# Optimization experiments

Hardware: AMD Instinct MI355X
Metric: run time of the kernel (lower is better)

## Reference

```python
import jax, jax.numpy as jnp
import numpy as np

N, H, W, C = 8, 64, 64, 256
GC = 8            # channels per group (gc)
G = C // GC       # groups = 32
K = 3             # deformable kernel size
KK = K * K
DK = 3            # depthwise kernel size for offset/mask branch


def setup_inputs() -> dict:
    key = jax.random.key(0)
    ks = jax.random.split(key, 6)
    s = 0.02
    return {
        "x": jax.random.normal(ks[0], (N, H, W, C), jnp.float32),
        "dw_w": jax.random.normal(ks[1], (DK, DK, 1, C), jnp.float32) * s,
        "dw_b": jnp.zeros((C,), jnp.float32),
        "om_w": jax.random.normal(ks[2], (C, G * KK * 3), jnp.float32) * s,
        "om_b": jnp.zeros((G * KK * 3,), jnp.float32),
        "vp_w": jax.random.normal(ks[3], (C, C), jnp.float32) * s,
        "vp_b": jnp.zeros((C,), jnp.float32),
        "op_w": jax.random.normal(ks[4], (C, C), jnp.float32) * s,  # output_bias=False
    }


def _dcnv4(x, dw_w, dw_b, om_w, om_b, vp_w, vp_b, op_w):
    n, h, w, c = x.shape
    # --- offset/mask branch: depthwise conv then pointwise linear ---
    xdw = jax.lax.conv_general_dilated(
        x, dw_w, window_strides=(1, 1), padding="SAME",
        dimension_numbers=("NHWC", "HWIO", "NHWC"), feature_group_count=c) + dw_b
    om = (xdw @ om_w + om_b).reshape(n, h, w, G, KK * 3)
    offset = om[..., : 2 * KK].reshape(n, h, w, G, KK, 2)  # (dx, dy) per point
    mask = om[..., 2 * KK :]                                # [n,h,w,G,KK], raw (no softmax in v4)

    # --- value projection ---
    value = (x @ vp_w + vp_b).reshape(n, h, w, G, GC)

    # --- sampling locations: pixel + kernel-grid point + learned offset ---
    kg = (jnp.arange(K) - (K - 1) // 2).astype(jnp.float32)
    ky = jnp.repeat(kg, K)   # [KK]
    kx = jnp.tile(kg, K)     # [KK]
    base_y = jnp.arange(h, dtype=jnp.float32).reshape(1, h, 1, 1, 1)
    base_x = jnp.arange(w, dtype=jnp.float32).reshape(1, 1, w, 1, 1)
    py = base_y + ky + offset[..., 1]  # [n,h,w,G,KK]
    px = base_x + kx + offset[..., 0]

    y0 = jnp.floor(py)
    x0 = jnp.floor(px)
    ty = py - y0
    tx = px - x0

    n_idx = jnp.arange(n).reshape(n, 1, 1, 1, 1)
    g_idx = jnp.arange(G).reshape(1, 1, 1, G, 1)

    def gather(yi, xi):
        valid = (yi >= 0) & (yi <= h - 1) & (xi >= 0) & (xi <= w - 1)
        yc = jnp.clip(yi, 0, h - 1).astype(jnp.int32)
        xc = jnp.clip(xi, 0, w - 1).astype(jnp.int32)
        v = value[n_idx, yc, xc, g_idx]          # [n,h,w,G,KK,GC]
        return v * valid[..., None].astype(value.dtype)

    v00 = gather(y0, x0)
    v01 = gather(y0, x0 + 1)
    v10 = gather(y0 + 1, x0)
    v11 = gather(y0 + 1, x0 + 1)

    sampled = ((1 - ty) * (1 - tx))[..., None] * v00 \
            + ((1 - ty) * tx)[..., None] * v01 \
            + (ty * (1 - tx))[..., None] * v10 \
            + (ty * tx)[..., None] * v11        # [n,h,w,G,KK,GC]

    out = jnp.einsum("nhwgkc,nhwgk->nhwgc", sampled, mask).reshape(n, h, w, c)
    return out @ op_w                            # output proj, no bias


def reference(x, dw_w, dw_b, om_w, om_b, vp_w, vp_b, op_w):
    return _dcnv4(x, dw_w, dw_b, om_w, om_b, vp_w, vp_b, op_w)
```

## Files before the change

kernel.cpp:

```cpp
#include <hip/hip_runtime.h>


typedef __bf16 bf16_t;
typedef bf16_t bf16x8 __attribute__((ext_vector_type(8)));
typedef bf16_t bf16x4 __attribute__((ext_vector_type(4)));
typedef float f32x4 __attribute__((ext_vector_type(4)));

namespace {
constexpr int NN = 8, HH = 64, WW = 64, CC = 256;
constexpr int G = 32, GC = 8;
constexpr int NPIX = NN * HH * WW;
}

__device__ __forceinline__ size_t fragIdx(int row, int c) {
  return ((size_t)(row >> 4) * 4096) + ((c >> 5) * 512) + (((c >> 3) & 3) * 128) +
         ((row & 15) * 8) + (c & 7);
}

__global__ __launch_bounds__(256) void convert_weights_kernel(
    const float* __restrict__ om_w, const float* __restrict__ vp_w,
    const float* __restrict__ op_w, bf16_t* __restrict__ om_wG,
    bf16_t* __restrict__ vp_wF, bf16_t* __restrict__ op_wF) {
  __shared__ float s_t[64][65];
  __shared__ float s_w[256][27];
  const int b = blockIdx.x, t = threadIdx.x;
  if (b < 32) {
    const float* src;
    bf16_t* dst;
    int kt, nt;
    if (b < 16) { src = vp_w; dst = vp_wF; kt = b >> 2; nt = b & 3; }
    else        { src = op_w; dst = op_wF; kt = (b - 16) >> 2; nt = (b - 16) & 3; }
    const int nl = t & 63, kh = t >> 6;
    const int n = nt * 64 + nl;
#pragma unroll
    for (int i = 0; i < 16; ++i) {
      const int kl = kh * 16 + i;
      s_t[kl][nl] = src[(size_t)(kt * 64 + kl) * CC + n];
    }
    __syncthreads();
    const int lane = t & 63, kq = lane >> 4, n15 = lane & 15, n16 = t >> 6;
#pragma unroll
    for (int it = 0; it < 2; ++it) {
      bf16x8 v;
#pragma unroll
      for (int j = 0; j < 8; ++j)
        v[j] = (bf16_t)s_t[it * 32 + kq * 8 + j][n16 * 16 + n15];
      const size_t off = (size_t)(nt * 4 + n16) * 4096 + (size_t)(kt * 2 + it) * 512 +
                         kq * 128 + n15 * 8;
      *(bf16x8*)(dst + off) = v;
    }
  } else {
    const int g = b - 32;
#pragma unroll
    for (int j = 0; j < 27; ++j) s_w[t][j] = om_w[(size_t)t * 864 + g * 27 + j];
    __syncthreads();
#pragma unroll
    for (int i = 0; i < 4; ++i) {
      const int chunk = i * 256 + t;
      const int tile = chunk >> 9, ks = (chunk >> 6) & 7, kq = (chunk >> 4) & 3,
                n15 = chunk & 15;
      const int j = tile * 16 + n15;
      bf16x8 v;
#pragma unroll
      for (int cl = 0; cl < 8; ++cl) {
        const int c = ks * 32 + kq * 8 + cl;
        v[cl] = (j < 27) ? (bf16_t)s_w[c][j] : (bf16_t)0.0f;
      }
      *(bf16x8*)(om_wG + ((size_t)g << 13) + (size_t)chunk * 8) = v;
    }
  }
}

__global__ __launch_bounds__(512, 4) void dwconv_value_kernel(
    const float* __restrict__ x, const float* __restrict__ dw_w,
    const float* __restrict__ dw_b, const bf16_t* __restrict__ vp_wF,
    const float* __restrict__ vp_b, bf16_t* __restrict__ xdwF,
    bf16_t* __restrict__ value_g) {
  __shared__ bf16_t s_xf[64 * 256];

  const int t = threadIdx.x;
  const int row = blockIdx.x;
  const int y = row & 63;
  const int img = row >> 6;

  {
    const int cq = (t & 63) * 4;
    const int seg = t >> 6;
    const bool up = (y > 0), dn = (y < HH - 1);
    const float* xrow = x + (size_t)row * WW * CC + cq;

    const float4 bias = *(const float4*)&dw_b[cq];
    float4 dw[9];
#pragma unroll
    for (int i = 0; i < 9; ++i) dw[i] = *(const float4*)&dw_w[(size_t)i * CC + cq];

    const float4 zero = make_float4(0.f, 0.f, 0.f, 0.f);
    auto loadcol = [&](int xx, float4 c[3]) {
      if (xx < 0 || xx >= WW) { c[0] = c[1] = c[2] = zero; return; }
      c[0] = up ? *(const float4*)(xrow + ((size_t)xx - WW) * CC) : zero;
      c[1] = *(const float4*)(xrow + (size_t)xx * CC);
      c[2] = dn ? *(const float4*)(xrow + ((size_t)xx + WW) * CC) : zero;
    };

    const int x0 = seg * 8;
    float4 cm[3], cc[3], cp[3];
    loadcol(x0 - 1, cm);
    loadcol(x0, cc);

    for (int xx = x0; xx < x0 + 8; ++xx) {
      loadcol(xx + 1, cp);
      float4 a = bias;
#pragma unroll
      for (int r = 0; r < 3; ++r) {
        const float4 w0 = dw[r * 3 + 0], w1 = dw[r * 3 + 1], w2 = dw[r * 3 + 2];
        a.x = fmaf(cm[r].x, w0.x, fmaf(cc[r].x, w1.x, fmaf(cp[r].x, w2.x, a.x)));
        a.y = fmaf(cm[r].y, w0.y, fmaf(cc[r].y, w1.y, fmaf(cp[r].y, w2.y, a.y)));
        a.z = fmaf(cm[r].z, w0.z, fmaf(cc[r].z, w1.z, fmaf(cp[r].z, w2.z, a.z)));
        a.w = fmaf(cm[r].w, w0.w, fmaf(cc[r].w, w1.w, fmaf(cp[r].w, w2.w, a.w)));
      }
      const int pix = row * WW + xx;
      bf16x4 av, cv;
      av[0] = (bf16_t)a.x; av[1] = (bf16_t)a.y; av[2] = (bf16_t)a.z; av[3] = (bf16_t)a.w;
      cv[0] = (bf16_t)cc[1].x; cv[1] = (bf16_t)cc[1].y;
      cv[2] = (bf16_t)cc[1].z; cv[3] = (bf16_t)cc[1].w;
      *(bf16x4*)&xdwF[fragIdx(pix, cq)] = av;
      const int lf = (xx >> 4) * 4096 + ((cq >> 5) * 512) + (((cq >> 3) & 3) * 128) +
                     ((xx & 15) * 8) + (cq & 7);
      *(bf16x4*)&s_xf[lf] = cv;
#pragma unroll
      for (int r = 0; r < 3; ++r) { cm[r] = cc[r]; cc[r] = cp[r]; }
    }
  }
  __syncthreads();

  {
    const int lane = t & 63;
    const int wave = t >> 6;
    const int mq = wave >> 1;
    const int nh = wave & 1;
    const int m = lane & 15;
    const int kq = lane >> 4;

    const bf16_t* Ap = s_xf + mq * 4096 + lane * 8;
    const bf16_t* Bp = vp_wF + (size_t)(nh * 8) * 4096 + lane * 8;

    f32x4 acc[8] = {};
#pragma unroll
    for (int ks = 0; ks < 8; ++ks) {
      const bf16x8 a = *(const bf16x8*)(Ap + ks * 512);
#pragma unroll
      for (int i = 0; i < 8; ++i) {
        const bf16x8 b = *(const bf16x8*)(Bp + (size_t)i * 4096 + ks * 512);
        acc[i] = __builtin_amdgcn_mfma_f32_16x16x32_bf16(a, b, acc[i], 0, 0, 0);
      }
    }

#pragma unroll
    for (int i = 0; i < 8; ++i) {
      const int n = (nh * 8 + i) * 16 + m;
      const float bs = vp_b[n];
      const int g = n >> 3, c = n & 7;
      bf16_t* plane = value_g + ((size_t)(img * G + g) << 15) + c;
#pragma unroll
      for (int r = 0; r < 4; ++r) {
        const int pl = mq * 16 + kq * 4 + r;
        const int pin = y * 64 + pl;
        plane[(size_t)pin * GC] = (bf16_t)(acc[i][r] + bs);
      }
    }
  }
}

__global__ __launch_bounds__(512, 2) void oms_kernel(
    const bf16_t* __restrict__ xdwF, const bf16_t* __restrict__ om_wG,
    const float* __restrict__ om_b, const bf16_t* __restrict__ value_g,
    bf16_t* __restrict__ sampledF) {
  __shared__ bf16x8 s_v[66 * 66];
  __shared__ bf16_t s_om[8][4][128][8];

  const int t = threadIdx.x;
  const int lane = t & 63, wave = t >> 6;
  const int b = blockIdx.x;
  const int img = b & 7, g = (b >> 3) & 31, quarter = b >> 8;
  const int c15 = lane & 15, kq = lane >> 4;
  const int tile0 = img * 256 + quarter * 64;

  bf16x8 wf[2][8];
  {
    const bf16_t* base = om_wG + ((size_t)g << 13) + (size_t)lane * 8;
#pragma unroll
    for (int n2 = 0; n2 < 2; ++n2)
#pragma unroll
      for (int ks = 0; ks < 8; ++ks)
        wf[n2][ks] = *(const bf16x8*)(base + n2 * 4096 + ks * 512);
  }
  float bias[2][4];
#pragma unroll
  for (int n2 = 0; n2 < 2; ++n2)
#pragma unroll
    for (int r = 0; r < 4; ++r) {
      const int j = n2 * 16 + kq * 4 + r;
      bias[n2][r] = (j < 27) ? om_b[g * 27 + j] : 0.0f;
    }

  {
    const bf16x8 zv = {};
    for (int i = t; i < 260; i += 512) {
      int Y, X;
      if (i < 66)       { Y = 0;           X = i; }
      else if (i < 132) { Y = 65;          X = i - 66; }
      else if (i < 196) { Y = i - 132 + 1; X = 0; }
      else              { Y = i - 196 + 1; X = 65; }
      s_v[Y * 66 + X] = zv;
    }
    const bf16x8* plane = (const bf16x8*)(value_g + ((size_t)(img * G + g) << 15));
#pragma unroll
    for (int i = 0; i < 8; ++i) {
      const int c = i * 512 + t;
      s_v[((c >> 6) + 1) * 66 + (c & 63) + 1] = plane[c];
    }
  }

  {
    const int tb = tile0 + wave * 8;
#pragma unroll
    for (int q = 0; q < 8; ++q) {
      const bf16_t* Ap = xdwF + ((size_t)(tb + q)) * 4096 + (size_t)lane * 8;
      f32x4 a0 = {}, a1 = {};
#pragma unroll
      for (int ks = 0; ks < 8; ++ks) {
        const bf16x8 xf = *(const bf16x8*)(Ap + ks * 512);
        a0 = __builtin_amdgcn_mfma_f32_16x16x32_bf16(wf[0][ks], xf, a0, 0, 0, 0);
        a1 = __builtin_amdgcn_mfma_f32_16x16x32_bf16(wf[1][ks], xf, a1, 0, 0, 0);
      }
      const int p = q * 16 + c15;
      bf16x4 b0, b1;
#pragma unroll
      for (int r = 0; r < 4; ++r) {
        b0[r] = (bf16_t)(a0[r] + bias[0][r]);
        b1[r] = (bf16_t)(a1[r] + bias[1][r]);
      }
      *(bf16x4*)&s_om[wave][kq >> 1][p][(kq & 1) * 4] = b0;
      *(bf16x4*)&s_om[wave][2 + (kq >> 1)][p][(kq & 1) * 4] = b1;
    }
  }
  __syncthreads();

  {
    const int pinA = quarter * 1024 + wave * 128 + lane;
    const int pinB = pinA + 64;
    float arrA[27], arrB[27];
#pragma unroll
    for (int c = 0; c < 4; ++c) {
      const bf16x8 oA = *(const bf16x8*)&s_om[wave][c][lane][0];
      const bf16x8 oB = *(const bf16x8*)&s_om[wave][c][64 + lane][0];
#pragma unroll
      for (int j = 0; j < 8; ++j) {
        const int idx = c * 8 + j;
        if (idx < 27) { arrA[idx] = (float)oA[j]; arrB[idx] = (float)oB[j]; }
      }
    }
    const int xw = lane;
    const int yA = (pinA >> 6) & 63;
    const int yB = yA + 1;

    float accA[GC], accB[GC];
#pragma unroll
    for (int c = 0; c < GC; ++c) { accA[c] = 0.0f; accB[c] = 0.0f; }

    auto tap = [&](const float* arr, const int y, float* acc, const int k) {
      const float pxf = (float)(xw + (k % 3) - 1) + arr[2 * k];
      const float pyf = (float)(y + (k / 3) - 1) + arr[2 * k + 1];
      const float mk = arr[18 + k];
      const float x0f = floorf(pxf), y0f = floorf(pyf);
      const float tx = pxf - x0f, ty = pyf - y0f;
      const int ix = (int)x0f, iy = (int)y0f;

      const int iX0 = min(max(ix, -1), 64) + 1;
      const int iX1 = min(max(ix + 1, -1), 64) + 1;
      const int iY0 = min(max(iy, -1), 64) + 1;
      const int iY1 = min(max(iy + 1, -1), 64) + 1;

      const bf16x8 v00 = s_v[iY0 * 66 + iX0];
      const bf16x8 v01 = s_v[iY0 * 66 + iX1];
      const bf16x8 v10 = s_v[iY1 * 66 + iX0];
      const bf16x8 v11 = s_v[iY1 * 66 + iX1];

      const float w00 = mk * (1.0f - ty) * (1.0f - tx);
      const float w01 = mk * (1.0f - ty) * tx;
      const float w10 = mk * ty * (1.0f - tx);
      const float w11 = mk * ty * tx;

#pragma unroll
      for (int c = 0; c < GC; ++c) {
        float s = acc[c];
        s = fmaf(w00, (float)v00[c], s);
        s = fmaf(w01, (float)v01[c], s);
        s = fmaf(w10, (float)v10[c], s);
        s = fmaf(w11, (float)v11[c], s);
        acc[c] = s;
      }
    };

#pragma unroll
    for (int k = 0; k < 9; ++k) {
      tap(arrA, yA, accA, k);
      tap(arrB, yB, accB, k);
    }

    bf16x8 svA, svB;
#pragma unroll
    for (int c = 0; c < GC; ++c) {
      svA[c] = (bf16_t)accA[c];
      svB[c] = (bf16_t)accB[c];
    }
    *(bf16x8*)(sampledF + fragIdx(img * 4096 + pinA, g * 8)) = svA;
    *(bf16x8*)(sampledF + fragIdx(img * 4096 + pinB, g * 8)) = svB;
  }
}

__global__ __launch_bounds__(1024, 1) void out_gemm_kernel(
    const bf16_t* __restrict__ AF, const bf16_t* __restrict__ BF,
    float* __restrict__ out) {
  __shared__ bf16_t s_b[CC * CC];

  const int t = threadIdx.x;
  {
    const bf16x8* src = (const bf16x8*)BF;
    bf16x8* dst = (bf16x8*)s_b;
#pragma unroll
    for (int i = 0; i < 8; ++i) dst[i * 1024 + t] = src[i * 1024 + t];
  }
  __syncthreads();

  const int lane = t & 63;
  const int wave = t >> 6;
  const int mq = wave >> 1;
  const int nh = wave & 1;
  const int mt = blockIdx.x * 8 + mq;
  const int m = lane & 15;
  const int kq = lane >> 4;

  const bf16_t* Ap = AF + (size_t)mt * 4096 + lane * 8;
  const bf16_t* Bp = s_b + (size_t)(nh * 8) * 4096 + lane * 8;

  f32x4 acc[8] = {};
#pragma unroll
  for (int ks = 0; ks < 8; ++ks) {
    const bf16x8 a = *(const bf16x8*)(Ap + ks * 512);
#pragma unroll
    for (int i = 0; i < 8; ++i) {
      const bf16x8 b = *(const bf16x8*)(Bp + (size_t)i * 4096 + ks * 512);
      acc[i] = __builtin_amdgcn_mfma_f32_16x16x32_bf16(a, b, acc[i], 0, 0, 0);
    }
  }

#pragma unroll
  for (int i = 0; i < 8; ++i) {
    const int n = (nh * 8 + i) * 16 + m;
#pragma unroll
    for (int r = 0; r < 4; ++r) {
      const int pix = mt * 16 + kq * 4 + r;
      out[(size_t)pix * CC + n] = acc[i][r];
    }
  }
}

extern "C" void kernel_launch(void* const* d_in, const int* in_sizes, int n_in,
                              void* d_out, int out_size, void* d_ws, size_t ws_size,
                              hipStream_t stream) {
  const float* x = (const float*)d_in[0];
  const float* dw_w = (const float*)d_in[1];
  const float* dw_b = (const float*)d_in[2];
  const float* om_w = (const float*)d_in[3];
  const float* om_b = (const float*)d_in[4];
  const float* vp_w = (const float*)d_in[5];
  const float* vp_b = (const float*)d_in[6];
  const float* op_w = (const float*)d_in[7];
  float* out = (float*)d_out;

  char* ws = (char*)d_ws;
  bf16_t* value_g = (bf16_t*)ws;
  bf16_t* xdwF = (bf16_t*)(ws + 16777216);
  bf16_t* sampledF = (bf16_t*)(ws + 33554432);
  bf16_t* om_wG = (bf16_t*)(ws + 50331648);
  bf16_t* vp_wF = (bf16_t*)(ws + 50855936);
  bf16_t* op_wF = (bf16_t*)(ws + 50987008);

  convert_weights_kernel<<<64, 256, 0, stream>>>(om_w, vp_w, op_w,
                                                 om_wG, vp_wF, op_wF);
  dwconv_value_kernel<<<NN * HH, 512, 0, stream>>>(x, dw_w, dw_b, vp_wF, vp_b,
                                                   xdwF, value_g);
  oms_kernel<<<1024, 512, 0, stream>>>(xdwF, om_wG, om_b, value_g, sampledF);
  out_gemm_kernel<<<NPIX / 128, 1024, 0, stream>>>(sampledF, op_wF, out);
}
```

Before: 193.8 us.

## Stage dwconv and value outputs in shared memory for coalesced 16-byte stores

Instead of scattering 8-byte xdwF writes and 2-byte strided value_g writes straight to global memory, the kernel stages both results in LDS, using a rotated per-group layout to avoid bank conflicts. It then writes them out with contiguous bf16x8 stores. This is meant to cut uncoalesced global write traffic. In exchange it doubles the LDS footprint, drops the occupancy hint from 4 to 2 blocks, and adds extra barriers.

```diff
diff --git a/kernel.cpp b/kernel.cpp
--- a/kernel.cpp
+++ b/kernel.cpp
@@ -71,12 +71,13 @@
   }
 }
 
-__global__ __launch_bounds__(512, 4) void dwconv_value_kernel(
+__global__ __launch_bounds__(512, 2) void dwconv_value_kernel(
     const float* __restrict__ x, const float* __restrict__ dw_w,
     const float* __restrict__ dw_b, const bf16_t* __restrict__ vp_wF,
     const float* __restrict__ vp_b, bf16_t* __restrict__ xdwF,
     bf16_t* __restrict__ value_g) {
   __shared__ bf16_t s_xf[64 * 256];
+  __shared__ bf16_t s_xdw[64 * 256];
 
   const int t = threadIdx.x;
   const int row = blockIdx.x;
@@ -118,20 +119,29 @@
         a.z = fmaf(cm[r].z, w0.z, fmaf(cc[r].z, w1.z, fmaf(cp[r].z, w2.z, a.z)));
         a.w = fmaf(cm[r].w, w0.w, fmaf(cc[r].w, w1.w, fmaf(cp[r].w, w2.w, a.w)));
       }
-      const int pix = row * WW + xx;
       bf16x4 av, cv;
       av[0] = (bf16_t)a.x; av[1] = (bf16_t)a.y; av[2] = (bf16_t)a.z; av[3] = (bf16_t)a.w;
       cv[0] = (bf16_t)cc[1].x; cv[1] = (bf16_t)cc[1].y;
       cv[2] = (bf16_t)cc[1].z; cv[3] = (bf16_t)cc[1].w;
-      *(bf16x4*)&xdwF[fragIdx(pix, cq)] = av;
       const int lf = (xx >> 4) * 4096 + ((cq >> 5) * 512) + (((cq >> 3) & 3) * 128) +
                      ((xx & 15) * 8) + (cq & 7);
+      *(bf16x4*)&s_xdw[lf] = av;
       *(bf16x4*)&s_xf[lf] = cv;
 #pragma unroll
       for (int r = 0; r < 3; ++r) { cm[r] = cc[r]; cc[r] = cp[r]; }
     }
   }
   __syncthreads();
+
+  {
+    const bf16x8* src = (const bf16x8*)s_xdw;
+    bf16x8* dst = (bf16x8*)(xdwF + (size_t)row * 16384);
+#pragma unroll
+    for (int i = 0; i < 4; ++i) {
+      const int idx = i * 512 + t;
+      dst[idx] = src[idx];
+    }
+  }
 
   {
     const int lane = t & 63;
@@ -155,18 +165,32 @@
       }
     }
 
+    __syncthreads();
+
+    bf16_t* s_out = s_xf;
 #pragma unroll
     for (int i = 0; i < 8; ++i) {
       const int n = (nh * 8 + i) * 16 + m;
       const float bs = vp_b[n];
       const int g = n >> 3, c = n & 7;
-      bf16_t* plane = value_g + ((size_t)(img * G + g) << 15) + c;
 #pragma unroll
       for (int r = 0; r < 4; ++r) {
         const int pl = mq * 16 + kq * 4 + r;
-        const int pin = y * 64 + pl;
-        plane[(size_t)pin * GC] = (bf16_t)(acc[i][r] + bs);
-      }
+        s_out[pl * 256 + (((g + pl) & 31) << 3) + c] = (bf16_t)(acc[i][r] + bs);
+      }
+    }
+  }
+  __syncthreads();
+
+  {
+    const bf16x8* s16 = (const bf16x8*)s_xf;
+    bf16x8* dst = (bf16x8*)value_g;
+#pragma unroll
+    for (int i = 0; i < 4; ++i) {
+      const int chunk = i * 512 + t;
+      const int g = chunk >> 6, px = chunk & 63;
+      const bf16x8 v = s16[px * 32 + ((g + px) & 31)];
+      dst[((size_t)(img * G + g) << 12) + y * 64 + px] = v;
     }
   }
 }
```

Result: faster. 188.1 us (-3.0%).
